# Kernel optimization log

Measured on AMD Instinct MI355X. Metric: run time of the kernel, lower is better.

The kernel has to match this reference:

```python
import jax, jax.numpy as jnp
import numpy as np

K = 12           # boundary_k
TEMP = 0.75      # logit_temperature


def _knn_idx(p):
    # p: [N,3]; brute-force kNN within one batch element (pointops offsets => per-batch)
    sq = jnp.sum(p * p, axis=-1)
    d2 = sq[:, None] + sq[None, :] - 2.0 * (p @ p.T)   # [N,N]
    _, idx = jax.lax.top_k(-d2, K + 1)                  # self is nearest (d=0)
    return idx[:, 1:]                                    # drop self -> [N,K]


def _mlp2(x, W1, b1, W2, b2, relu_out):
    h = jax.nn.relu(x @ W1 + b1) @ W2 + b2
    return jax.nn.relu(h) if relu_out else h


def setup_inputs() -> dict:
    key = jax.random.key(0)
    ks = jax.random.split(key, 32)
    B, N, C = 4, 4096, 17
    dims = [256, 512, 768]
    RD = 320
    s = 0.02
    inp = {
        'feat0': jax.random.normal(ks[0], (B, N, dims[0]), jnp.float32),
        'feat1': jax.random.normal(ks[1], (B, N, dims[1]), jnp.float32),
        'feat2': jax.random.normal(ks[2], (B, N, dims[2]), jnp.float32),
        'logits': jax.random.normal(ks[3], (B, N, C), jnp.float32),
        'labels': jax.random.randint(ks[4], (B, N), 0, C, jnp.int32),
        'pos': jax.random.normal(ks[5], (B, N, 3), jnp.float32),
    }
    # feat projections
    for i, d in enumerate(dims):
        inp[f'Wp{i}'] = jax.random.normal(ks[6 + i], (d, RD), jnp.float32) * s
        inp[f'bp{i}'] = jnp.zeros((RD,), jnp.float32)
    # boundary encoder 6->96->160
    inp['Wbe1'] = jax.random.normal(ks[10], (6, 96), jnp.float32) * s
    inp['bbe1'] = jnp.zeros((96,), jnp.float32)
    inp['Wbe2'] = jax.random.normal(ks[11], (96, 160), jnp.float32) * s
    inp['bbe2'] = jnp.zeros((160,), jnp.float32)
    # attention (RD+160)->320->n_scales
    inp['Wa1'] = jax.random.normal(ks[12], (RD + 160, 320), jnp.float32) * s
    inp['ba1'] = jnp.zeros((320,), jnp.float32)
    inp['Wa2'] = jax.random.normal(ks[13], (320, 3), jnp.float32) * s
    inp['ba2'] = jnp.zeros((3,), jnp.float32)
    # output proj RD->RD->RD
    inp['Wo1'] = jax.random.normal(ks[14], (RD, RD), jnp.float32) * s
    inp['bo1'] = jnp.zeros((RD,), jnp.float32)
    inp['Wo2'] = jax.random.normal(ks[15], (RD, RD), jnp.float32) * s
    inp['bo2'] = jnp.zeros((RD,), jnp.float32)
    return inp


def boundary_info(logits, labels, pos):
    idx = jax.vmap(_knn_idx)(pos)                          # [B,N,K]
    nb_lab = jax.vmap(lambda l, i: l[i])(labels, idx)      # [B,N,K]
    nb_pos = jax.vmap(lambda p, i: p[i])(pos, idx)         # [B,N,K,3]
    diff = nb_lab != labels[..., None]                     # [B,N,K]
    diff_f = diff.astype(jnp.float32)
    dist = jnp.linalg.norm(nb_pos - pos[:, :, None, :], axis=-1)  # [B,N,K]
    boundary_score = diff_f.mean(axis=-1)
    same = 1.0 - diff_f
    same_dist = (dist * same).sum(-1) / (same.sum(-1) + 1e-6)
    bdist = jnp.min(jnp.where(diff, dist, jnp.inf), axis=-1)
    bdist = jnp.where(jnp.isfinite(bdist), bdist, same_dist)
    mean_d = dist.mean(-1)
    density = 1.0 / (mean_d + 1e-6)
    curvature = jnp.std(dist, axis=-1, ddof=1) / (mean_d + 1e-6)  # torch.std unbiased
    probs = jax.nn.softmax(logits / TEMP, axis=-1)
    confidence = probs.max(-1)
    entropy = -(probs * jnp.log(probs + 1e-8)).sum(-1) / jnp.log(jnp.float32(probs.shape[-1]))
    return jnp.stack([boundary_score, confidence, entropy, density, curvature, bdist], axis=-1)


def reference(feat0, feat1, feat2, logits, labels, pos,
              Wp0, bp0, Wp1, bp1, Wp2, bp2,
              Wbe1, bbe1, Wbe2, bbe2,
              Wa1, ba1, Wa2, ba2,
              Wo1, bo1, Wo2, bo2):
    fp = jnp.stack([feat0 @ Wp0 + bp0, feat1 @ Wp1 + bp1, feat2 @ Wp2 + bp2], axis=2)  # [B,N,3,RD]
    info = boundary_info(logits, labels, pos)                       # [B,N,6]
    enc = _mlp2(info, Wbe1, bbe1, Wbe2, bbe2, relu_out=True)        # [B,N,160]
    global_feat = fp.mean(axis=2)                                   # [B,N,RD]
    attn_in = jnp.concatenate([global_feat, enc], axis=-1)
    attn = jax.nn.softmax(_mlp2(attn_in, Wa1, ba1, Wa2, ba2, relu_out=False), axis=-1)  # [B,N,3]
    fused = (fp * attn[..., None]).sum(axis=2)                      # [B,N,RD]
    out = _mlp2(fused, Wo1, bo1, Wo2, bo2, relu_out=False) + global_feat
    return out, attn
```

## Files before the change

kernel.cpp:

```cpp
#include <hip/hip_runtime.h>
#include <stdint.h>

typedef float fx4 __attribute__((ext_vector_type(4)));
typedef short s8 __attribute__((ext_vector_type(8)));
typedef short s4 __attribute__((ext_vector_type(4)));
typedef unsigned int u32;
typedef u32 ux4 __attribute__((ext_vector_type(4)));

#define MTOT 16384
#define NPTS 4096

#define VMCNT7 asm volatile("s_waitcnt vmcnt(7)" ::: "memory")
#define VMCNT5 asm volatile("s_waitcnt vmcnt(5)" ::: "memory")
#define VMCNT0 asm volatile("s_waitcnt vmcnt(0)" ::: "memory")
#define LGKM0  asm volatile("s_waitcnt lgkmcnt(0)" ::: "memory")
#define SBAR   asm volatile("s_barrier" ::: "memory")
#define SCHED0 __builtin_amdgcn_sched_barrier(0)

__device__ __forceinline__ float b2f(short s) {
    return __uint_as_float(((unsigned)(unsigned short)s) << 16);
}
__device__ __forceinline__ short f2b(float f) {
    unsigned u = __float_as_uint(f);
    u += 0x7fffu + ((u >> 16) & 1u);
    return (short)(u >> 16);
}
__device__ __forceinline__ void g2l16(const void* g, void* l) {
    __builtin_amdgcn_global_load_lds(
        (const __attribute__((address_space(1))) unsigned int*)g,
        (__attribute__((address_space(3))) unsigned int*)l, 16, 0, 0);
}
__device__ __forceinline__ void g2l4(const void* g, void* l) {
    __builtin_amdgcn_global_load_lds(
        (const __attribute__((address_space(1))) unsigned int*)g,
        (__attribute__((address_space(3))) unsigned int*)l, 4, 0, 0);
}

struct WTDesc {
    const float* W[8];
    short* Bt[8];
    int K[8];
    int N[8];
    int Kp[8];
    int swz[8];
    int base[9];
};

__global__ __launch_bounds__(256) void wtrans8_kernel(WTDesc d)
{
    int idx = blockIdx.x * 256 + threadIdx.x;
    if (idx >= d.base[8]) return;
    int s = 0;
#pragma unroll
    for (int t = 1; t < 8; ++t) if (idx >= d.base[t]) s = t;
    int local = idx - d.base[s];
    int N = d.N[s];
    if (d.swz[s]) {
        int c = local / 10240, r = local - c * 10240;
        int n = r >> 5, q = r & 31, slot = q >> 3, t = q & 7;
        int kl = ((slot ^ ((n >> 1) & 3)) << 3) | t;
        int k = c * 32 + kl;
        d.Bt[s][local] = f2b(d.W[s][(size_t)k * N + n]);
    } else {
        int Kp = d.Kp[s], K = d.K[s];
        int n = local / Kp, k = local - n * Kp;
        d.Bt[s][local] = (k < K) ? f2b(d.W[s][(size_t)k * N + n]) : (short)0;
    }
}

#define SEGW 132
#define KCAP 40

template<int K>
__device__ __forceinline__ void aprep_one(
    const float* __restrict__ src, short* __restrict__ dst, int aid)
{
    constexpr int KT8 = K * 4;
    int mtile = aid / KT8;
    int r8 = aid - mtile * KT8;
    int r2 = r8 * 8;
    int chunk = r2 >> 10;
    int within = r2 & 1023;
    int r = within >> 5, q = within & 31;
    int slot = q >> 3;
    int k = chunk * 32 + ((slot ^ ((r >> 1) & 3)) << 3);
    int row = mtile * 32 + r;
    const float* sp = src + (size_t)row * K + k;
    fx4 v0 = *(const fx4*)sp, v1 = *(const fx4*)(sp + 4);
    s8 o;
    o[0] = f2b(v0[0]); o[1] = f2b(v0[1]); o[2] = f2b(v0[2]); o[3] = f2b(v0[3]);
    o[4] = f2b(v1[0]); o[5] = f2b(v1[1]); o[6] = f2b(v1[2]); o[7] = f2b(v1[3]);
    *(s8*)(dst + (size_t)aid * 8) = o;
}

__global__ __launch_bounds__(512) void knap_kernel(
    const float* __restrict__ pos, u32* __restrict__ keys,
    const float* __restrict__ f0, const float* __restrict__ f1, const float* __restrict__ f2,
    short* __restrict__ a0, short* __restrict__ a1, short* __restrict__ a2)
{
    __shared__ float xs[8 * SEGW], ys[8 * SEGW], zs[8 * SEGW];
    __shared__ u32 cand[64 * KCAP];
    __shared__ u32 samp[64 * 16];
    __shared__ u32 tauA[64];
    __shared__ int cnt[64];

    int bid = blockIdx.x;
    if (bid >= 1024) {
        int g = (bid - 1024) * 512 + threadIdx.x;
        if (g < 1572864)      aprep_one<768>(f2, a2, g);
        else if (g < 2621440) aprep_one<512>(f1, a1, g - 1572864);
        else                  aprep_one<256>(f0, a0, g - 2621440);
        return;
    }

    int b   = bid >> 8;
    int cc  = (bid >> 6) & 3;
    int pch = bid & 63;
    int tid = threadIdx.x;
    int jb  = cc << 10;

    if (tid < 64) cnt[tid] = 0;
    for (int idx = tid; idx < 1024; idx += 512) {
        int seg = idx >> 7, o = idx & 127;
        const float* pp = pos + (size_t)(b * NPTS + jb + idx) * 3;
        xs[seg * SEGW + o] = pp[0];
        ys[seg * SEGW + o] = pp[1];
        zs[seg * SEGW + o] = pp[2];
    }
    __syncthreads();

    int lp = tid >> 3, q = tid & 7;
    int gi = pch * 64 + lp;
    const float* mp = pos + (size_t)(b * NPTS + gi) * 3;
    float mx = mp[0], my = mp[1], mz = mp[2];

    const float* xsq = xs + q * SEGW;
    const float* ysq = ys + q * SEGW;
    const float* zsq = zs + q * SEGW;
    int jg0 = jb + q * 128;

    u32 h0 = 0xFFFFFFFFu, h1v = 0xFFFFFFFFu;
    for (int jj = 0; jj < 128; jj += 4) {
        fx4 xv = *reinterpret_cast<const fx4*>(xsq + jj);
        fx4 yv = *reinterpret_cast<const fx4*>(ysq + jj);
        fx4 zv = *reinterpret_cast<const fx4*>(zsq + jj);
#pragma unroll
        for (int u = 0; u < 4; ++u) {
            float dx = xv[u] - mx, dy = yv[u] - my, dz = zv[u] - mz;
            float d2 = fmaf(dx, dx, fmaf(dy, dy, dz * dz));
            u32 d2m = __float_as_uint(d2) & 0xFFFFF000u;
            if (jg0 + jj + u == gi) d2m = 0xFFFFFFFFu;
            u32 lo = (d2m < h0) ? d2m : h0;
            u32 hi = (d2m < h0) ? h0 : d2m;
            h0 = lo;
            h1v = (hi < h1v) ? hi : h1v;
        }
    }
    u32 m0 = h0 | (u32)(q * 2);
    u32 m1 = h1v | (u32)(q * 2 + 1);
    samp[lp * 16 + q * 2]     = m0;
    samp[lp * 16 + q * 2 + 1] = m1;
    __syncthreads();

    {
        ux4 sv0 = *(ux4*)&samp[lp * 16];
        ux4 sv1 = *(ux4*)&samp[lp * 16 + 4];
        ux4 sv2 = *(ux4*)&samp[lp * 16 + 8];
        ux4 sv3 = *(ux4*)&samp[lp * 16 + 12];
        int r0 = 0, r1 = 0;
#pragma unroll
        for (int i = 0; i < 4; ++i) {
            r0 += (sv0[i] < m0) + (sv1[i] < m0) + (sv2[i] < m0) + (sv3[i] < m0);
            r1 += (sv0[i] < m1) + (sv1[i] < m1) + (sv2[i] < m1) + (sv3[i] < m1);
        }
        if (r0 == 11) tauA[lp] = m0;
        if (r1 == 11) tauA[lp] = m1;
    }
    __syncthreads();
    u32 tau = tauA[lp];

    for (int jj = 0; jj < 128; jj += 4) {
        fx4 xv = *reinterpret_cast<const fx4*>(xsq + jj);
        fx4 yv = *reinterpret_cast<const fx4*>(ysq + jj);
        fx4 zv = *reinterpret_cast<const fx4*>(zsq + jj);
#pragma unroll
        for (int u = 0; u < 4; ++u) {
            float dx = xv[u] - mx, dy = yv[u] - my, dz = zv[u] - mz;
            float d2 = fmaf(dx, dx, fmaf(dy, dy, dz * dz));
            int jg = jg0 + jj + u;
            u32 d2m = __float_as_uint(d2) & 0xFFFFF000u;
            if (jg == gi) d2m = 0xFFFFFFFFu;
            if (d2m <= tau) {
                int slot = atomicAdd(&cnt[lp], 1);
                if (slot < KCAP) cand[lp * KCAP + slot] = d2m | (u32)jg;
            }
        }
    }
    __syncthreads();

    int n = cnt[lp];
    u32 out[12];
    if (n <= KCAP) {
        u32 e0, e1, e2, e3, e4;
        e0 = (q      < n) ? cand[lp * KCAP + q]      : 0xFFFFFFFFu;
        e1 = (q + 8  < n) ? cand[lp * KCAP + q + 8]  : 0xFFFFFFFFu;
        e2 = (q + 16 < n) ? cand[lp * KCAP + q + 16] : 0xFFFFFFFFu;
        e3 = (q + 24 < n) ? cand[lp * KCAP + q + 24] : 0xFFFFFFFFu;
        e4 = (q + 32 < n) ? cand[lp * KCAP + q + 32] : 0xFFFFFFFFu;
#define CE(a, b) { u32 t0 = (a < b) ? a : b; u32 t1 = (a < b) ? b : a; a = t0; b = t1; }
        CE(e0, e1) CE(e1, e2) CE(e2, e3) CE(e3, e4)
        CE(e0, e1) CE(e1, e2) CE(e2, e3)
        CE(e0, e1) CE(e1, e2)
        CE(e0, e1)
#undef CE
        cand[lp * KCAP + q]      = e0;
        cand[lp * KCAP + q + 8]  = e1;
        cand[lp * KCAP + q + 16] = e2;
        cand[lp * KCAP + q + 24] = e3;
        cand[lp * KCAP + q + 32] = e4;
        int ptr = 0;
        u32 head = e0;
#pragma unroll
        for (int r = 0; r < 12; ++r) {
            u32 m = head;
            u32 o1 = __shfl_xor(m, 4, 8); m = (o1 < m) ? o1 : m;
            u32 o2 = __shfl_xor(m, 2, 8); m = (o2 < m) ? o2 : m;
            u32 o3 = __shfl_xor(m, 1, 8); m = (o3 < m) ? o3 : m;
            if (m == head) {
                ++ptr;
                head = (ptr < 5) ? cand[lp * KCAP + q + ptr * 8] : 0xFFFFFFFFu;
            }
            out[r] = m;
        }
    } else {
        u32 hk[12];
#pragma unroll
        for (int k = 0; k < 12; ++k) hk[k] = 0xFFFFFFFFu;
        for (int jj = 0; jj < 128; jj += 4) {
            fx4 xv = *reinterpret_cast<const fx4*>(xsq + jj);
            fx4 yv = *reinterpret_cast<const fx4*>(ysq + jj);
            fx4 zv = *reinterpret_cast<const fx4*>(zsq + jj);
#pragma unroll
            for (int u = 0; u < 4; ++u) {
                float dx = xv[u] - mx, dy = yv[u] - my, dz = zv[u] - mz;
                float d2 = fmaf(dx, dx, fmaf(dy, dy, dz * dz));
                int jg = jg0 + jj + u;
                u32 key = (__float_as_uint(d2) & 0xFFFFF000u) | (u32)jg;
                if (jg == gi) key = 0xFFFFFFFFu;
                if (key < hk[11]) {
                    hk[11] = key;
#pragma unroll
                    for (int k = 11; k >= 1; --k) {
                        u32 a = hk[k], bb = hk[k - 1];
                        u32 mn = (a < bb) ? a : bb;
                        u32 mxv = (a < bb) ? bb : a;
                        hk[k - 1] = mn; hk[k] = mxv;
                    }
                }
            }
        }
#pragma unroll
        for (int r = 0; r < 12; ++r) {
            u32 m = hk[0];
            u32 o1 = __shfl_xor(m, 4, 8); m = (o1 < m) ? o1 : m;
            u32 o2 = __shfl_xor(m, 2, 8); m = (o2 < m) ? o2 : m;
            u32 o3 = __shfl_xor(m, 1, 8); m = (o3 < m) ? o3 : m;
            if (m == hk[0]) {
#pragma unroll
                for (int k = 0; k < 11; ++k) hk[k] = hk[k + 1];
                hk[11] = 0xFFFFFFFFu;
            }
            out[r] = m;
        }
    }

    size_t kb = ((size_t)(b * NPTS + gi) * 4 + cc) * 12;
    if (q == 0) *reinterpret_cast<ux4*>(&keys[kb])     = (ux4){out[0], out[1], out[2], out[3]};
    if (q == 1) *reinterpret_cast<ux4*>(&keys[kb + 4]) = (ux4){out[4], out[5], out[6], out[7]};
    if (q == 2) *reinterpret_cast<ux4*>(&keys[kb + 8]) = (ux4){out[8], out[9], out[10], out[11]};
}

__global__ __launch_bounds__(256) void knn_merge_kernel(
    const u32* __restrict__ keys, const int* __restrict__ labels,
    const float* __restrict__ logits, float* __restrict__ info32)
{
    __shared__ unsigned char labs[NPTS];
    int b  = blockIdx.x >> 6;
    int pc = blockIdx.x & 63;
    int tid = threadIdx.x;
    for (int idx = tid; idx < NPTS; idx += 256)
        labs[idx] = (unsigned char)labels[b * NPTS + idx];
    __syncthreads();

    int lp = tid >> 2, q = tid & 3;
    int gi = pc * 64 + lp;
    size_t kb = ((size_t)(b * NPTS + gi) * 4 + q) * 12;
    ux4 k0 = *reinterpret_cast<const ux4*>(&keys[kb]);
    ux4 k1 = *reinterpret_cast<const ux4*>(&keys[kb + 4]);
    ux4 k2 = *reinterpret_cast<const ux4*>(&keys[kb + 8]);
    u32 hk[12];
    hk[0] = k0[0]; hk[1] = k0[1]; hk[2] = k0[2]; hk[3] = k0[3];
    hk[4] = k1[0]; hk[5] = k1[1]; hk[6] = k1[2]; hk[7] = k1[3];
    hk[8] = k2[0]; hk[9] = k2[1]; hk[10] = k2[2]; hk[11] = k2[3];

    int mylab = (int)labs[gi];
    float sum_d = 0.f, sum_d2 = 0.f, sum_diff = 0.f, same_d = 0.f, bmin = 3.0e38f;
#pragma unroll
    for (int r = 0; r < 12; ++r) {
        u32 m = hk[0];
        u32 o1 = __shfl_xor(m, 2, 4); m = (o1 < m) ? o1 : m;
        u32 o2 = __shfl_xor(m, 1, 4); m = (o2 < m) ? o2 : m;
        if (m == hk[0]) {
#pragma unroll
            for (int k = 0; k < 11; ++k) hk[k] = hk[k + 1];
            hk[11] = 0xFFFFFFFFu;
        }
        float d = sqrtf(__uint_as_float(m & 0xFFFFF000u));
        int j = (int)(m & 0xFFFu);
        float isdiff = ((int)labs[j] != mylab) ? 1.0f : 0.0f;
        sum_d += d;
        sum_d2 = fmaf(d, d, sum_d2);
        sum_diff += isdiff;
        same_d = fmaf(d, 1.0f - isdiff, same_d);
        if (isdiff > 0.f) bmin = fminf(bmin, d);
    }

    if (q == 0) {
        float nsame = 12.0f - sum_diff;
        float mean_d = sum_d * (1.0f / 12.0f);
        float var = fmaxf(0.f, (sum_d2 - 12.0f * mean_d * mean_d) * (1.0f / 11.0f));
        float md_eps = mean_d + 1e-6f;
        float curvature = sqrtf(var) / md_eps;
        float density = 1.0f / md_eps;
        float same_dist = same_d / (nsame + 1e-6f);
        float bdist = (bmin < 2.9e38f) ? bmin : same_dist;
        float bscore = sum_diff * (1.0f / 12.0f);

        const float* lg = logits + (size_t)(b * NPTS + gi) * 17;
        float v[17];
        float vmax = -3.0e38f;
#pragma unroll
        for (int c = 0; c < 17; ++c) { v[c] = lg[c] * (1.0f / 0.75f); vmax = fmaxf(vmax, v[c]); }
        float ssum = 0.f;
#pragma unroll
        for (int c = 0; c < 17; ++c) { v[c] = expf(v[c] - vmax); ssum += v[c]; }
        float inv = 1.0f / ssum;
        float conf = 0.f, ent = 0.f;
#pragma unroll
        for (int c = 0; c < 17; ++c) {
            float pprob = v[c] * inv;
            conf = fmaxf(conf, pprob);
            ent += pprob * logf(pprob + 1e-8f);
        }
        ent = -ent * (1.0f / 2.8332133f);

        float* op = info32 + (size_t)(b * NPTS + gi) * 32;
        fx4 o0 = {bscore, conf, ent, density};
        fx4 o1v = {curvature, bdist, 0.f, 0.f};
        fx4 zz = {0.f, 0.f, 0.f, 0.f};
        *reinterpret_cast<fx4*>(op + 0)  = o0;
        *reinterpret_cast<fx4*>(op + 4)  = o1v;
        *reinterpret_cast<fx4*>(op + 8)  = zz;
        *reinterpret_cast<fx4*>(op + 12) = zz;
        *reinterpret_cast<fx4*>(op + 16) = zz;
        *reinterpret_cast<fx4*>(op + 20) = zz;
        *reinterpret_cast<fx4*>(op + 24) = zz;
        *reinterpret_cast<fx4*>(op + 28) = zz;
    }
}

template<bool AF32, bool RELU, bool NMASK, bool ADDF, bool OUTF, bool OUTB>
__global__ __launch_bounds__(256) void gemm_k(
    const void* __restrict__ Ap, int lda,
    const short* __restrict__ Bt,
    const float* __restrict__ bias,
    float* __restrict__ Cf, int ldcf,
    short* __restrict__ Cb, int ldcb, int cboff,
    const float* __restrict__ Af, int ldaf,
    int N, int K, int ntiles)
{
    __shared__ short As[128 * 40];
    __shared__ short Bs[64 * 40];
    int bid = blockIdx.x;
    int mt = bid / ntiles, nt = bid - mt * ntiles;
    int m0 = mt * 128, n0 = nt * 64;
    int tid = threadIdx.x, l = tid & 63, wid = tid >> 6;
    int wm = wid & 1, wn = wid >> 1, lr = l & 15, lh = l >> 4;
    fx4 acc[4][2] = {};

    int nsteps = K >> 5;
    for (int kt = 0; kt < nsteps; ++kt) {
        int k0 = kt << 5;
        if constexpr (AF32) {
            const float* A = (const float*)Ap;
#pragma unroll
            for (int it = 0; it < 4; ++it) {
                int tt = tid + it * 256;
                int row = tt >> 3, seg = tt & 7;
                fx4 vv = *reinterpret_cast<const fx4*>(A + (size_t)(m0 + row) * lda + k0 + seg * 4);
                s4 w; w[0] = f2b(vv[0]); w[1] = f2b(vv[1]); w[2] = f2b(vv[2]); w[3] = f2b(vv[3]);
                *reinterpret_cast<s4*>(&As[row * 40 + seg * 4]) = w;
            }
        } else {
            const short* A = (const short*)Ap;
#pragma unroll
            for (int it = 0; it < 2; ++it) {
                int tt = tid + it * 256;
                int row = tt >> 2, seg = tt & 3;
                s8 vv = *reinterpret_cast<const s8*>(A + (size_t)(m0 + row) * lda + k0 + seg * 8);
                *reinterpret_cast<s8*>(&As[row * 40 + seg * 8]) = vv;
            }
        }
        {
            int row = tid >> 2, seg = tid & 3;
            s8 vb = {0, 0, 0, 0, 0, 0, 0, 0};
            if (!NMASK || (n0 + row) < N)
                vb = *reinterpret_cast<const s8*>(Bt + (size_t)(n0 + row) * K + k0 + seg * 8);
            *reinterpret_cast<s8*>(&Bs[row * 40 + seg * 8]) = vb;
        }
        __syncthreads();
        s8 af[4], bfr[2];
#pragma unroll
        for (int mf = 0; mf < 4; ++mf)
            af[mf] = *reinterpret_cast<s8*>(&As[(wm * 64 + mf * 16 + lr) * 40 + lh * 8]);
#pragma unroll
        for (int nf = 0; nf < 2; ++nf)
            bfr[nf] = *reinterpret_cast<s8*>(&Bs[(wn * 32 + nf * 16 + lr) * 40 + lh * 8]);
#pragma unroll
        for (int mf = 0; mf < 4; ++mf)
#pragma unroll
            for (int nf = 0; nf < 2; ++nf)
                acc[mf][nf] = __builtin_amdgcn_mfma_f32_16x16x32_bf16(af[mf], bfr[nf], acc[mf][nf], 0, 0, 0);
        __syncthreads();
    }

#pragma unroll
    for (int nf = 0; nf < 2; ++nf) {
        int col = n0 + wn * 32 + nf * 16 + lr;
        if (NMASK && col >= N) continue;
        float bv = bias[col];
#pragma unroll
        for (int mf = 0; mf < 4; ++mf) {
            int r0 = m0 + wm * 64 + mf * 16 + lh * 4;
#pragma unroll
            for (int rg = 0; rg < 4; ++rg) {
                float c = acc[mf][nf][rg] + bv;
                if (RELU) c = fmaxf(c, 0.0f);
                int row = r0 + rg;
                if constexpr (ADDF) c += Af[(size_t)row * ldaf + col];
                if constexpr (OUTF) Cf[(size_t)row * ldcf + col] = c;
                if constexpr (OUTB) Cb[(size_t)row * ldcb + cboff + col] = f2b(c);
            }
        }
    }
}

__global__ __launch_bounds__(256, 2) void mega_kernel(
    const short* __restrict__ at0, const short* __restrict__ at1, const short* __restrict__ at2,
    const short* __restrict__ btp0, const short* __restrict__ btp1, const short* __restrict__ btp2,
    const float* __restrict__ bp0, const float* __restrict__ bp1, const float* __restrict__ bp2,
    const short* __restrict__ bta1, const float* __restrict__ ba1,
    const float* __restrict__ Wa2, const float* __restrict__ ba2,
    const short* __restrict__ bto1, const float* __restrict__ bo1,
    const short* __restrict__ bto2, const float* __restrict__ bo2,
    const short* __restrict__ encb, short* __restrict__ fpb,
    float* __restrict__ outf, float* __restrict__ attn_out)
{
    __shared__ alignas(16) short smem[38144];
    char* smb = (char*)smem;
    constexpr int BB0 = 0, BB1 = 20480, AB0 = 40960, AB1 = 43008, R2B = 45056, SWF = 75776;
    constexpr size_t FPS = (size_t)512 * 256 * 40;
    float* smf = (float*)(smb + SWF);

    int tid = threadIdx.x, l = tid & 63, wid = tid >> 6;
    int lr = l & 15, lh = l >> 4;
    int m0 = blockIdx.x * 32;
    short* fpt = fpb + (size_t)(blockIdx.x * 256 + tid) * 40;

    auto stageB = [&](int bbase, const short* btg, int kt) {
#pragma unroll
        for (int r = 0; r < 5; ++r) {
            int idx = tid + r * 256;
            g2l16(btg + (size_t)kt * 10240 + idx * 8, smb + bbase + idx * 16);
        }
    };
    auto stageA = [&](int abase, const short* atgm, int kt) {
        const short* src = atgm + (size_t)kt * 1024;
        g2l4(src + tid * 2,       smb + abase + tid * 4);
        g2l4(src + 512 + tid * 2, smb + abase + 1024 + tid * 4);
    };
    auto readB = [&](int bbase, s8* bf) {
#pragma unroll
        for (int nf = 0; nf < 5; ++nf) {
            int row = wid * 80 + nf * 16 + lr;
            bf[nf] = *(const s8*)(smb + bbase + row * 64 + ((lh ^ ((row >> 1) & 3)) << 4));
        }
    };
    auto readAp = [&](int abase, s8* af) {
#pragma unroll
        for (int mf = 0; mf < 2; ++mf) {
            int row = mf * 16 + lr;
            af[mf] = *(const s8*)(smb + abase + row * 64 + ((lh ^ ((row >> 1) & 3)) << 4));
        }
    };

    fx4 gacc[2][5] = {};

    auto do_proj = [&](const short* atgm, const short* btg, int ns,
                       const float* bias, short* fpo) {
        fx4 acc[2][5] = {};
        stageB(BB0, btg, 0); stageA(AB0, atgm, 0);
        stageB(BB1, btg, 1); stageA(AB1, atgm, 1);
        LGKM0;
#pragma unroll 1
        for (int kt = 0; kt < ns; ++kt) {
            if (kt < ns - 1) { VMCNT7; } else { VMCNT0; }
            SBAR;
            int cb = (kt & 1) ? BB1 : BB0;
            int ca = (kt & 1) ? AB1 : AB0;
            s8 af[2], bf[5];
            readAp(ca, af);
            readB(cb, bf);
            LGKM0; SCHED0;
            SBAR;
            if (kt + 2 < ns) { stageB(cb, btg, kt + 2); stageA(ca, atgm, kt + 2); }
#pragma unroll
            for (int mf = 0; mf < 2; ++mf)
#pragma unroll
                for (int nf = 0; nf < 5; ++nf)
                    acc[mf][nf] = __builtin_amdgcn_mfma_f32_16x16x32_bf16(af[mf], bf[nf], acc[mf][nf], 0, 0, 0);
        }
#pragma unroll
        for (int nf = 0; nf < 5; ++nf) {
            float bv = bias[wid * 80 + nf * 16 + lr];
#pragma unroll
            for (int mf = 0; mf < 2; ++mf) {
                s4 pk;
#pragma unroll
                for (int rg = 0; rg < 4; ++rg) {
                    float c = acc[mf][nf][rg] + bv;
                    gacc[mf][nf][rg] += c;
                    pk[rg] = f2b(c);
                }
                *(s4*)(fpo + (mf * 5 + nf) * 4) = pk;
            }
        }
    };

    do_proj(at2 + (size_t)blockIdx.x * 24576, btp2, 24, bp2, fpt + 2 * FPS);
    do_proj(at1 + (size_t)blockIdx.x * 16384, btp1, 16, bp1, fpt + 1 * FPS);
    do_proj(at0 + (size_t)blockIdx.x * 8192,  btp0, 8,  bp0, fpt);

#pragma unroll
    for (int nf = 0; nf < 5; ++nf) {
        int col = wid * 80 + nf * 16 + lr;
#pragma unroll
        for (int mf = 0; mf < 2; ++mf)
#pragma unroll
            for (int rg = 0; rg < 4; ++rg) {
                int row = mf * 16 + lh * 4 + rg;
                int bir = (col * 2) ^ (((row >> 1) & 3) << 4);
                *(short*)(smb + R2B + row * 960 + bir) = f2b(gacc[mf][nf][rg] * (1.0f / 3.0f));
            }
    }
#pragma unroll
    for (int r = 0; r < 3; ++r) {
        int idx = tid + r * 256;
        if (idx < 640) {
            int row = idx / 20, sg = idx - row * 20;
            s8 v = *reinterpret_cast<const s8*>(encb + (size_t)(m0 + row) * 160 + sg * 8);
            int bir = (640 + sg * 16) ^ (((row >> 1) & 3) << 4);
            *(s8*)(smb + R2B + row * 960 + bir) = v;
        }
    }

    auto do_gemm2 = [&](const short* btg, int ns, fx4 (&acc)[2][5]) {
        stageB(BB0, btg, 0);
        stageB(BB1, btg, 1);
        LGKM0;
#pragma unroll 1
        for (int kt = 0; kt < ns; ++kt) {
            if (kt < ns - 1) { VMCNT5; } else { VMCNT0; }
            SBAR;
            int cb = (kt & 1) ? BB1 : BB0;
            s8 af[2], bf[5];
#pragma unroll
            for (int mf = 0; mf < 2; ++mf) {
                int row = mf * 16 + lr;
                int bir = (kt * 64 + (lh << 4)) ^ (((row >> 1) & 3) << 4);
                af[mf] = *(const s8*)(smb + R2B + row * 960 + bir);
            }
            readB(cb, bf);
            LGKM0; SCHED0;
            SBAR;
            if (kt + 2 < ns) stageB(cb, btg, kt + 2);
#pragma unroll
            for (int mf = 0; mf < 2; ++mf)
#pragma unroll
                for (int nf = 0; nf < 5; ++nf)
                    acc[mf][nf] = __builtin_amdgcn_mfma_f32_16x16x32_bf16(af[mf], bf[nf], acc[mf][nf], 0, 0, 0);
        }
    };

    {
        fx4 acc1[2][5] = {};
        do_gemm2(bta1, 15, acc1);
#pragma unroll
        for (int nf = 0; nf < 5; ++nf) {
            int col = wid * 80 + nf * 16 + lr;
            float bv = ba1[col];
#pragma unroll
            for (int mf = 0; mf < 2; ++mf)
#pragma unroll
                for (int rg = 0; rg < 4; ++rg) {
                    int row = mf * 16 + lh * 4 + rg;
                    int bir = (col * 2) ^ (((row >> 1) & 3) << 4);
                    *(short*)(smb + R2B + row * 960 + bir) = f2b(fmaxf(acc1[mf][nf][rg] + bv, 0.0f));
                }
        }
    }

    {
        float* ws2 = (float*)smb;
        if (tid < 240)
            reinterpret_cast<fx4*>(ws2)[tid] = reinterpret_cast<const fx4*>(Wa2)[tid];
        __syncthreads();
        int row = tid >> 3, g = tid & 7;
        float l0 = 0.f, l1 = 0.f, l2 = 0.f;
#pragma unroll
        for (int j = 0; j < 5; ++j) {
            int bir = (g * 80 + j * 16) ^ (((row >> 1) & 3) << 4);
            s8 v = *(const s8*)(smb + R2B + row * 960 + bir);
#pragma unroll
            for (int u = 0; u < 8; ++u) {
                float f = b2f(v[u]);
                const float* wp = ws2 + (g * 40 + j * 8 + u) * 3;
                l0 = fmaf(f, wp[0], l0);
                l1 = fmaf(f, wp[1], l1);
                l2 = fmaf(f, wp[2], l2);
            }
        }
#pragma unroll
        for (int s = 4; s >= 1; s >>= 1) {
            l0 += __shfl_xor(l0, s, 8);
            l1 += __shfl_xor(l1, s, 8);
            l2 += __shfl_xor(l2, s, 8);
        }
        if (g == 0) {
            l0 += ba2[0]; l1 += ba2[1]; l2 += ba2[2];
            float mx = fmaxf(l0, fmaxf(l1, l2));
            float e0 = expf(l0 - mx), e1 = expf(l1 - mx), e2 = expf(l2 - mx);
            float inv = 1.0f / (e0 + e1 + e2);
            float w0 = e0 * inv, w1 = e1 * inv, w2 = e2 * inv;
            attn_out[(size_t)(m0 + row) * 3 + 0] = w0;
            attn_out[(size_t)(m0 + row) * 3 + 1] = w1;
            attn_out[(size_t)(m0 + row) * 3 + 2] = w2;
            smf[row * 4 + 0] = w0; smf[row * 4 + 1] = w1; smf[row * 4 + 2] = w2;
        }
        __syncthreads();
    }

#pragma unroll
    for (int mf = 0; mf < 2; ++mf)
#pragma unroll
        for (int nf = 0; nf < 5; ++nf) {
            s4 p0 = *(const s4*)(fpt + (mf * 5 + nf) * 4);
            s4 p1 = *(const s4*)(fpt + 1 * FPS + (mf * 5 + nf) * 4);
            s4 p2 = *(const s4*)(fpt + 2 * FPS + (mf * 5 + nf) * 4);
            int col = wid * 80 + nf * 16 + lr;
#pragma unroll
            for (int rg = 0; rg < 4; ++rg) {
                int row = mf * 16 + lh * 4 + rg;
                float fv = smf[row * 4 + 0] * b2f(p0[rg])
                         + smf[row * 4 + 1] * b2f(p1[rg])
                         + smf[row * 4 + 2] * b2f(p2[rg]);
                int bir = (col * 2) ^ (((row >> 1) & 3) << 4);
                *(short*)(smb + R2B + row * 960 + bir) = f2b(fv);
            }
        }

    {
        fx4 acch[2][5] = {};
        do_gemm2(bto1, 10, acch);
#pragma unroll
        for (int nf = 0; nf < 5; ++nf) {
            int col = wid * 80 + nf * 16 + lr;
            float bv = bo1[col];
#pragma unroll
            for (int mf = 0; mf < 2; ++mf)
#pragma unroll
                for (int rg = 0; rg < 4; ++rg) {
                    int row = mf * 16 + lh * 4 + rg;
                    int bir = (col * 2) ^ (((row >> 1) & 3) << 4);
                    *(short*)(smb + R2B + row * 960 + bir) = f2b(fmaxf(acch[mf][nf][rg] + bv, 0.0f));
                }
        }
    }

    {
        fx4 acco[2][5] = {};
        do_gemm2(bto2, 10, acco);
#pragma unroll
        for (int nf = 0; nf < 5; ++nf) {
            int col = wid * 80 + nf * 16 + lr;
            float bv = bo2[col];
#pragma unroll
            for (int mf = 0; mf < 2; ++mf)
#pragma unroll
                for (int rg = 0; rg < 4; ++rg) {
                    int row = m0 + mf * 16 + lh * 4 + rg;
                    float c = acco[mf][nf][rg] + bv + gacc[mf][nf][rg] * (1.0f / 3.0f);
                    outf[(size_t)row * 320 + col] = c;
                }
        }
    }
}

extern "C" void kernel_launch(void* const* d_in, const int* in_sizes, int n_in,
                              void* d_out, int out_size, void* d_ws, size_t ws_size,
                              hipStream_t stream)
{
    const float* feat0  = (const float*)d_in[0];
    const float* feat1  = (const float*)d_in[1];
    const float* feat2  = (const float*)d_in[2];
    const float* logits = (const float*)d_in[3];
    const int*   labels = (const int*)d_in[4];
    const float* pos    = (const float*)d_in[5];
    const float* Wp0 = (const float*)d_in[6];   const float* bp0 = (const float*)d_in[7];
    const float* Wp1 = (const float*)d_in[8];   const float* bp1 = (const float*)d_in[9];
    const float* Wp2 = (const float*)d_in[10];  const float* bp2 = (const float*)d_in[11];
    const float* Wbe1 = (const float*)d_in[12]; const float* bbe1 = (const float*)d_in[13];
    const float* Wbe2 = (const float*)d_in[14]; const float* bbe2 = (const float*)d_in[15];
    const float* Wa1 = (const float*)d_in[16];  const float* ba1 = (const float*)d_in[17];
    const float* Wa2 = (const float*)d_in[18];  const float* ba2 = (const float*)d_in[19];
    const float* Wo1 = (const float*)d_in[20];  const float* bo1 = (const float*)d_in[21];
    const float* Wo2 = (const float*)d_in[22];  const float* bo2 = (const float*)d_in[23];

    char* p = (char*)d_ws;
    auto alloc = [&](size_t bytes) { char* r = p; p += (bytes + 255) & ~(size_t)255; return r; };
    short* bt_p0  = (short*)alloc((size_t)320 * 256 * 2);
    short* bt_p1  = (short*)alloc((size_t)320 * 512 * 2);
    short* bt_p2  = (short*)alloc((size_t)320 * 768 * 2);
    short* bt_be1 = (short*)alloc((size_t)96 * 32 * 2);
    short* bt_be2 = (short*)alloc((size_t)160 * 96 * 2);
    short* bt_a1  = (short*)alloc((size_t)320 * 480 * 2);
    short* bt_o1  = (short*)alloc((size_t)320 * 320 * 2);
    short* bt_o2  = (short*)alloc((size_t)320 * 320 * 2);
    float* info32 = (float*)alloc((size_t)MTOT * 32 * 4);
    short* h1     = (short*)alloc((size_t)MTOT * 96 * 2);
    short* encb   = (short*)alloc((size_t)MTOT * 160 * 2);
    u32*   knnkeys= (u32*)alloc((size_t)MTOT * 4 * 12 * 4);
    short* abt0   = (short*)alloc((size_t)MTOT * 256 * 2);
    short* abt1   = (short*)alloc((size_t)MTOT * 512 * 2);
    short* abt2   = (short*)alloc((size_t)MTOT * 768 * 2);
    short* fpb    = (short*)alloc((size_t)3 * 512 * 256 * 40 * 2);

    float* outf = (float*)d_out;
    float* attn_out = outf + (size_t)MTOT * 320;

    WTDesc wd;
    const float* Ws[8] = {Wp0, Wp1, Wp2, Wbe1, Wbe2, Wa1, Wo1, Wo2};
    short* Bts[8] = {bt_p0, bt_p1, bt_p2, bt_be1, bt_be2, bt_a1, bt_o1, bt_o2};
    int Ks[8]  = {256, 512, 768, 6, 96, 480, 320, 320};
    int Ns[8]  = {320, 320, 320, 96, 160, 320, 320, 320};
    int Kps[8] = {256, 512, 768, 32, 96, 480, 320, 320};
    int Sz[8]  = {1, 1, 1, 0, 0, 1, 1, 1};
    int acc = 0;
    for (int s = 0; s < 8; ++s) {
        wd.W[s] = Ws[s]; wd.Bt[s] = Bts[s];
        wd.K[s] = Ks[s]; wd.N[s] = Ns[s]; wd.Kp[s] = Kps[s]; wd.swz[s] = Sz[s];
        wd.base[s] = acc;
        acc += Ns[s] * Kps[s];
    }
    wd.base[8] = acc;
    wtrans8_kernel<<<(acc + 255) / 256, 256, 0, stream>>>(wd);

    knap_kernel<<<7168, 512, 0, stream>>>(pos, knnkeys,
                                          feat0, feat1, feat2,
                                          abt0, abt1, abt2);
    knn_merge_kernel<<<256, 256, 0, stream>>>(knnkeys, labels, logits, info32);

    gemm_k<true, true, true, false, false, true><<<256, 256, 0, stream>>>(
        info32, 32, bt_be1, bbe1, nullptr, 0, h1, 96, 0, nullptr, 0, 96, 32, 2);
    gemm_k<false, true, true, false, false, true><<<384, 256, 0, stream>>>(
        h1, 96, bt_be2, bbe2, nullptr, 0, encb, 160, 0, nullptr, 0, 160, 96, 3);

    mega_kernel<<<512, 256, 0, stream>>>(
        abt0, abt1, abt2,
        bt_p0, bt_p1, bt_p2,
        bp0, bp1, bp2,
        bt_a1, ba1, Wa2, ba2,
        bt_o1, bo1, bt_o2, bo2,
        encb, fpb, outf, attn_out);
}
```

Measured before the change: 131.8 us.

## Use 512-thread blocks in mega_kernel with 2x4 warp tiling

Raises mega_kernel from 256 to 512 threads per block and arranges the 8 waves as 2 (M) x 4 (N), so each wave computes one 16-row fragment instead of two. The B and A staging loads are respread across the larger thread count, the vmcnt waits are adjusted to match, and the per-thread fp scratch layout shrinks to 20 shorts. The goal is more waves per CU to hide latency and fewer accumulator registers per thread. In exchange each wave does less MFMA work per LDS B-fragment read and the barriers cover more waves.

```diff
diff --git a/kernel.cpp b/kernel.cpp
--- a/kernel.cpp
+++ b/kernel.cpp
@@ -10,8 +10,8 @@
 #define MTOT 16384
 #define NPTS 4096
 
-#define VMCNT7 asm volatile("s_waitcnt vmcnt(7)" ::: "memory")
 #define VMCNT5 asm volatile("s_waitcnt vmcnt(5)" ::: "memory")
+#define VMCNT4 asm volatile("s_waitcnt vmcnt(4)" ::: "memory")
 #define VMCNT0 asm volatile("s_waitcnt vmcnt(0)" ::: "memory")
 #define LGKM0  asm volatile("s_waitcnt lgkmcnt(0)" ::: "memory")
 #define SBAR   asm volatile("s_barrier" ::: "memory")
@@ -455,7 +455,7 @@
     }
 }
 
-__global__ __launch_bounds__(256, 2) void mega_kernel(
+__global__ __launch_bounds__(512, 2) void mega_kernel(
     const short* __restrict__ at0, const short* __restrict__ at1, const short* __restrict__ at2,
     const short* __restrict__ btp0, const short* __restrict__ btp1, const short* __restrict__ btp2,
     const float* __restrict__ bp0, const float* __restrict__ bp1, const float* __restrict__ bp2,
@@ -469,154 +469,141 @@
     __shared__ alignas(16) short smem[38144];
     char* smb = (char*)smem;
     constexpr int BB0 = 0, BB1 = 20480, AB0 = 40960, AB1 = 43008, R2B = 45056, SWF = 75776;
-    constexpr size_t FPS = (size_t)512 * 256 * 40;
+    constexpr size_t FPS = (size_t)512 * 512 * 20;
     float* smf = (float*)(smb + SWF);
 
-    int tid = threadIdx.x, l = tid & 63, wid = tid >> 6;
-    int lr = l & 15, lh = l >> 4;
+    int tid = threadIdx.x, wid = tid >> 6, l = tid & 63;
+    int wm = wid >> 2, wn = wid & 3, lr = l & 15, lh = l >> 4;
     int m0 = blockIdx.x * 32;
-    short* fpt = fpb + (size_t)(blockIdx.x * 256 + tid) * 40;
+    short* fpt = fpb + (size_t)(blockIdx.x * 512 + tid) * 20;
 
     auto stageB = [&](int bbase, const short* btg, int kt) {
-#pragma unroll
-        for (int r = 0; r < 5; ++r) {
-            int idx = tid + r * 256;
-            g2l16(btg + (size_t)kt * 10240 + idx * 8, smb + bbase + idx * 16);
-        }
+        const char* s = (const char*)(btg + (size_t)kt * 10240);
+        int o1 = tid * 16;
+        int o2 = 8192 + tid * 16;
+        int o3 = 16384 + tid * 4;
+        int o4 = 18432 + tid * 4;
+        g2l16(s + o1, smb + bbase + o1);
+        g2l16(s + o2, smb + bbase + o2);
+        g2l4(s + o3, smb + bbase + o3);
+        g2l4(s + o4, smb + bbase + o4);
     };
     auto stageA = [&](int abase, const short* atgm, int kt) {
-        const short* src = atgm + (size_t)kt * 1024;
-        g2l4(src + tid * 2,       smb + abase + tid * 4);
-        g2l4(src + 512 + tid * 2, smb + abase + 1024 + tid * 4);
+        const char* s = (const char*)(atgm + (size_t)kt * 1024);
+        g2l4(s + tid * 4, smb + abase + tid * 4);
     };
     auto readB = [&](int bbase, s8* bf) {
 #pragma unroll
         for (int nf = 0; nf < 5; ++nf) {
-            int row = wid * 80 + nf * 16 + lr;
+            int row = wn * 80 + nf * 16 + lr;
             bf[nf] = *(const s8*)(smb + bbase + row * 64 + ((lh ^ ((row >> 1) & 3)) << 4));
         }
     };
-    auto readAp = [&](int abase, s8* af) {
-#pragma unroll
-        for (int mf = 0; mf < 2; ++mf) {
-            int row = mf * 16 + lr;
-            af[mf] = *(const s8*)(smb + abase + row * 64 + ((lh ^ ((row >> 1) & 3)) << 4));
-        }
-    };
-
-    fx4 gacc[2][5] = {};
+
+    fx4 gacc[5] = {};
 
     auto do_proj = [&](const short* atgm, const short* btg, int ns,
                        const float* bias, short* fpo) {
-        fx4 acc[2][5] = {};
+        fx4 acc[5] = {};
         stageB(BB0, btg, 0); stageA(AB0, atgm, 0);
         stageB(BB1, btg, 1); stageA(AB1, atgm, 1);
-        LGKM0;
-#pragma unroll 1
-        for (int kt = 0; kt < ns; ++kt) {
-            if (kt < ns - 1) { VMCNT7; } else { VMCNT0; }
-            SBAR;
-            int cb = (kt & 1) ? BB1 : BB0;
-            int ca = (kt & 1) ? AB1 : AB0;
-            s8 af[2], bf[5];
-            readAp(ca, af);
-            readB(cb, bf);
-            LGKM0; SCHED0;
-            SBAR;
-            if (kt + 2 < ns) { stageB(cb, btg, kt + 2); stageA(ca, atgm, kt + 2); }
-#pragma unroll
-            for (int mf = 0; mf < 2; ++mf)
-#pragma unroll
-                for (int nf = 0; nf < 5; ++nf)
-                    acc[mf][nf] = __builtin_amdgcn_mfma_f32_16x16x32_bf16(af[mf], bf[nf], acc[mf][nf], 0, 0, 0);
-        }
-#pragma unroll
-        for (int nf = 0; nf < 5; ++nf) {
-            float bv = bias[wid * 80 + nf * 16 + lr];
-#pragma unroll
-            for (int mf = 0; mf < 2; ++mf) {
-                s4 pk;
-#pragma unroll
-                for (int rg = 0; rg < 4; ++rg) {
-                    float c = acc[mf][nf][rg] + bv;
-                    gacc[mf][nf][rg] += c;
-                    pk[rg] = f2b(c);
-                }
-                *(s4*)(fpo + (mf * 5 + nf) * 4) = pk;
-            }
-        }
-    };
-
-    do_proj(at2 + (size_t)blockIdx.x * 24576, btp2, 24, bp2, fpt + 2 * FPS);
-    do_proj(at1 + (size_t)blockIdx.x * 16384, btp1, 16, bp1, fpt + 1 * FPS);
-    do_proj(at0 + (size_t)blockIdx.x * 8192,  btp0, 8,  bp0, fpt);
-
-#pragma unroll
-    for (int nf = 0; nf < 5; ++nf) {
-        int col = wid * 80 + nf * 16 + lr;
-#pragma unroll
-        for (int mf = 0; mf < 2; ++mf)
-#pragma unroll
-            for (int rg = 0; rg < 4; ++rg) {
-                int row = mf * 16 + lh * 4 + rg;
-                int bir = (col * 2) ^ (((row >> 1) & 3) << 4);
-                *(short*)(smb + R2B + row * 960 + bir) = f2b(gacc[mf][nf][rg] * (1.0f / 3.0f));
-            }
-    }
-#pragma unroll
-    for (int r = 0; r < 3; ++r) {
-        int idx = tid + r * 256;
-        if (idx < 640) {
-            int row = idx / 20, sg = idx - row * 20;
-            s8 v = *reinterpret_cast<const s8*>(encb + (size_t)(m0 + row) * 160 + sg * 8);
-            int bir = (640 + sg * 16) ^ (((row >> 1) & 3) << 4);
-            *(s8*)(smb + R2B + row * 960 + bir) = v;
-        }
-    }
-
-    auto do_gemm2 = [&](const short* btg, int ns, fx4 (&acc)[2][5]) {
-        stageB(BB0, btg, 0);
-        stageB(BB1, btg, 1);
         LGKM0;
 #pragma unroll 1
         for (int kt = 0; kt < ns; ++kt) {
             if (kt < ns - 1) { VMCNT5; } else { VMCNT0; }
             SBAR;
             int cb = (kt & 1) ? BB1 : BB0;
-            s8 af[2], bf[5];
-#pragma unroll
-            for (int mf = 0; mf < 2; ++mf) {
-                int row = mf * 16 + lr;
+            int ca = (kt & 1) ? AB1 : AB0;
+            s8 af, bf[5];
+            {
+                int row = wm * 16 + lr;
+                af = *(const s8*)(smb + ca + row * 64 + ((lh ^ ((row >> 1) & 3)) << 4));
+            }
+            readB(cb, bf);
+            LGKM0; SCHED0;
+            SBAR;
+            if (kt + 2 < ns) { stageB(cb, btg, kt + 2); stageA(ca, atgm, kt + 2); }
+#pragma unroll
+            for (int nf = 0; nf < 5; ++nf)
+                acc[nf] = __builtin_amdgcn_mfma_f32_16x16x32_bf16(af, bf[nf], acc[nf], 0, 0, 0);
+        }
+#pragma unroll
+        for (int nf = 0; nf < 5; ++nf) {
+            float bv = bias[wn * 80 + nf * 16 + lr];
+            s4 pk;
+#pragma unroll
+            for (int rg = 0; rg < 4; ++rg) {
+                float c = acc[nf][rg] + bv;
+                gacc[nf][rg] += c;
+                pk[rg] = f2b(c);
+            }
+            *(s4*)(fpo + nf * 4) = pk;
+        }
+    };
+
+    do_proj(at2 + (size_t)blockIdx.x * 24576, btp2, 24, bp2, fpt + 2 * FPS);
+    do_proj(at1 + (size_t)blockIdx.x * 16384, btp1, 16, bp1, fpt + 1 * FPS);
+    do_proj(at0 + (size_t)blockIdx.x * 8192,  btp0, 8,  bp0, fpt);
+
+#pragma unroll
+    for (int nf = 0; nf < 5; ++nf) {
+        int col = wn * 80 + nf * 16 + lr;
+#pragma unroll
+        for (int rg = 0; rg < 4; ++rg) {
+            int row = wm * 16 + lh * 4 + rg;
+            int bir = (col * 2) ^ (((row >> 1) & 3) << 4);
+            *(short*)(smb + R2B + row * 960 + bir) = f2b(gacc[nf][rg] * (1.0f / 3.0f));
+        }
+    }
+#pragma unroll
+    for (int r = 0; r < 2; ++r) {
+        int idx = tid + r * 512;
+        if (idx < 640) {
+            int row = idx / 20, sg = idx - row * 20;
+            s8 v = *reinterpret_cast<const s8*>(encb + (size_t)(m0 + row) * 160 + sg * 8);
+            int bir = (640 + sg * 16) ^ (((row >> 1) & 3) << 4);
+            *(s8*)(smb + R2B + row * 960 + bir) = v;
+        }
+    }
+
+    auto do_gemm2 = [&](const short* btg, int ns, fx4 (&acc)[5]) {
+        stageB(BB0, btg, 0);
+        stageB(BB1, btg, 1);
+        LGKM0;
+#pragma unroll 1
+        for (int kt = 0; kt < ns; ++kt) {
+            if (kt < ns - 1) { VMCNT4; } else { VMCNT0; }
+            SBAR;
+            int cb = (kt & 1) ? BB1 : BB0;
+            s8 af, bf[5];
+            {
+                int row = wm * 16 + lr;
                 int bir = (kt * 64 + (lh << 4)) ^ (((row >> 1) & 3) << 4);
-                af[mf] = *(const s8*)(smb + R2B + row * 960 + bir);
+                af = *(const s8*)(smb + R2B + row * 960 + bir);
             }
             readB(cb, bf);
             LGKM0; SCHED0;
             SBAR;
             if (kt + 2 < ns) stageB(cb, btg, kt + 2);
 #pragma unroll
-            for (int mf = 0; mf < 2; ++mf)
-#pragma unroll
-                for (int nf = 0; nf < 5; ++nf)
-                    acc[mf][nf] = __builtin_amdgcn_mfma_f32_16x16x32_bf16(af[mf], bf[nf], acc[mf][nf], 0, 0, 0);
+            for (int nf = 0; nf < 5; ++nf)
+                acc[nf] = __builtin_amdgcn_mfma_f32_16x16x32_bf16(af, bf[nf], acc[nf], 0, 0, 0);
         }
     };
 
     {
-        fx4 acc1[2][5] = {};
+        fx4 acc1[5] = {};
         do_gemm2(bta1, 15, acc1);
 #pragma unroll
         for (int nf = 0; nf < 5; ++nf) {
-            int col = wid * 80 + nf * 16 + lr;
+            int col = wn * 80 + nf * 16 + lr;
             float bv = ba1[col];
 #pragma unroll
-            for (int mf = 0; mf < 2; ++mf)
-#pragma unroll
-                for (int rg = 0; rg < 4; ++rg) {
-                    int row = mf * 16 + lh * 4 + rg;
-                    int bir = (col * 2) ^ (((row >> 1) & 3) << 4);
-                    *(short*)(smb + R2B + row * 960 + bir) = f2b(fmaxf(acc1[mf][nf][rg] + bv, 0.0f));
-                }
+            for (int rg = 0; rg < 4; ++rg) {
+                int row = wm * 16 + lh * 4 + rg;
+                int bir = (col * 2) ^ (((row >> 1) & 3) << 4);
+                *(short*)(smb + R2B + row * 960 + bir) = f2b(fmaxf(acc1[nf][rg] + bv, 0.0f));
+            }
         }
     }
 
@@ -625,93 +612,89 @@
         if (tid < 240)
             reinterpret_cast<fx4*>(ws2)[tid] = reinterpret_cast<const fx4*>(Wa2)[tid];
         __syncthreads();
-        int row = tid >> 3, g = tid & 7;
-        float l0 = 0.f, l1 = 0.f, l2 = 0.f;
-#pragma unroll
-        for (int j = 0; j < 5; ++j) {
-            int bir = (g * 80 + j * 16) ^ (((row >> 1) & 3) << 4);
-            s8 v = *(const s8*)(smb + R2B + row * 960 + bir);
-#pragma unroll
-            for (int u = 0; u < 8; ++u) {
-                float f = b2f(v[u]);
-                const float* wp = ws2 + (g * 40 + j * 8 + u) * 3;
-                l0 = fmaf(f, wp[0], l0);
-                l1 = fmaf(f, wp[1], l1);
-                l2 = fmaf(f, wp[2], l2);
-            }
-        }
-#pragma unroll
-        for (int s = 4; s >= 1; s >>= 1) {
-            l0 += __shfl_xor(l0, s, 8);
-            l1 += __shfl_xor(l1, s, 8);
-            l2 += __shfl_xor(l2, s, 8);
-        }
-        if (g == 0) {
-            l0 += ba2[0]; l1 += ba2[1]; l2 += ba2[2];
-            float mx = fmaxf(l0, fmaxf(l1, l2));
-            float e0 = expf(l0 - mx), e1 = expf(l1 - mx), e2 = expf(l2 - mx);
-            float inv = 1.0f / (e0 + e1 + e2);
-            float w0 = e0 * inv, w1 = e1 * inv, w2 = e2 * inv;
-            attn_out[(size_t)(m0 + row) * 3 + 0] = w0;
-            attn_out[(size_t)(m0 + row) * 3 + 1] = w1;
-            attn_out[(size_t)(m0 + row) * 3 + 2] = w2;
-            smf[row * 4 + 0] = w0; smf[row * 4 + 1] = w1; smf[row * 4 + 2] = w2;
+        if (tid < 256) {
+            int row = tid >> 3, g = tid & 7;
+            float l0 = 0.f, l1 = 0.f, l2 = 0.f;
+#pragma unroll
+            for (int j = 0; j < 5; ++j) {
+                int bir = (g * 80 + j * 16) ^ (((row >> 1) & 3) << 4);
+                s8 v = *(const s8*)(smb + R2B + row * 960 + bir);
+#pragma unroll
+                for (int u = 0; u < 8; ++u) {
+                    float f = b2f(v[u]);
+                    const float* wp = ws2 + (g * 40 + j * 8 + u) * 3;
+                    l0 = fmaf(f, wp[0], l0);
+                    l1 = fmaf(f, wp[1], l1);
+                    l2 = fmaf(f, wp[2], l2);
+                }
+            }
+#pragma unroll
+            for (int s = 4; s >= 1; s >>= 1) {
+                l0 += __shfl_xor(l0, s, 8);
+                l1 += __shfl_xor(l1, s, 8);
+                l2 += __shfl_xor(l2, s, 8);
+            }
+            if (g == 0) {
+                l0 += ba2[0]; l1 += ba2[1]; l2 += ba2[2];
+                float mx = fmaxf(l0, fmaxf(l1, l2));
+                float e0 = expf(l0 - mx), e1 = expf(l1 - mx), e2 = expf(l2 - mx);
+                float inv = 1.0f / (e0 + e1 + e2);
+                float w0 = e0 * inv, w1 = e1 * inv, w2 = e2 * inv;
+                attn_out[(size_t)(m0 + row) * 3 + 0] = w0;
+                attn_out[(size_t)(m0 + row) * 3 + 1] = w1;
+                attn_out[(size_t)(m0 + row) * 3 + 2] = w2;
+                smf[row * 4 + 0] = w0; smf[row * 4 + 1] = w1; smf[row * 4 + 2] = w2;
+            }
         }
         __syncthreads();
     }
 
 #pragma unroll
-    for (int mf = 0; mf < 2; ++mf)
+    for (int nf = 0; nf < 5; ++nf) {
+        s4 p0 = *(const s4*)(fpt + nf * 4);
+        s4 p1 = *(const s4*)(fpt + 1 * FPS + nf * 4);
+        s4 p2 = *(const s4*)(fpt + 2 * FPS + nf * 4);
+        int col = wn * 80 + nf * 16 + lr;
+#pragma unroll
+        for (int rg = 0; rg < 4; ++rg) {
+            int row = wm * 16 + lh * 4 + rg;
+            float fv = smf[row * 4 + 0] * b2f(p0[rg])
+                     + smf[row * 4 + 1] * b2f(p1[rg])
+                     + smf[row * 4 + 2] * b2f(p2[rg]);
+            int bir = (col * 2) ^ (((row >> 1) & 3) << 4);
+            *(short*)(smb + R2B + row * 960 + bir) = f2b(fv);
+        }
+    }
+
+    {
+        fx4 acch[5] = {};
+        do_gemm2(bto1, 10, acch);
 #pragma unroll
         for (int nf = 0; nf < 5; ++nf) {
-            s4 p0 = *(const s4*)(fpt + (mf * 5 + nf) * 4);
-            s4 p1 = *(const s4*)(fpt + 1 * FPS + (mf * 5 + nf) * 4);
-            s4 p2 = *(const s4*)(fpt + 2 * FPS + (mf * 5 + nf) * 4);
-            int col = wid * 80 + nf * 16 + lr;
+            int col = wn * 80 + nf * 16 + lr;
+            float bv = bo1[col];
 #pragma unroll
             for (int rg = 0; rg < 4; ++rg) {
-                int row = mf * 16 + lh * 4 + rg;
-                float fv = smf[row * 4 + 0] * b2f(p0[rg])
-                         + smf[row * 4 + 1] * b2f(p1[rg])
-                         + smf[row * 4 + 2] * b2f(p2[rg]);
+                int row = wm * 16 + lh * 4 + rg;
                 int bir = (col * 2) ^ (((row >> 1) & 3) << 4);
-                *(short*)(smb + R2B + row * 960 + bir) = f2b(fv);
-            }
-        }
+                *(short*)(smb + R2B + row * 960 + bir) = f2b(fmaxf(acch[nf][rg] + bv, 0.0f));
+            }
+        }
+    }
 
     {
-        fx4 acch[2][5] = {};
-        do_gemm2(bto1, 10, acch);
+        fx4 acco[5] = {};
+        do_gemm2(bto2, 10, acco);
 #pragma unroll
         for (int nf = 0; nf < 5; ++nf) {
-            int col = wid * 80 + nf * 16 + lr;
-            float bv = bo1[col];
-#pragma unroll
-            for (int mf = 0; mf < 2; ++mf)
-#pragma unroll
-                for (int rg = 0; rg < 4; ++rg) {
-                    int row = mf * 16 + lh * 4 + rg;
-                    int bir = (col * 2) ^ (((row >> 1) & 3) << 4);
-                    *(short*)(smb + R2B + row * 960 + bir) = f2b(fmaxf(acch[mf][nf][rg] + bv, 0.0f));
-                }
-        }
-    }
-
-    {
-        fx4 acco[2][5] = {};
-        do_gemm2(bto2, 10, acco);
-#pragma unroll
-        for (int nf = 0; nf < 5; ++nf) {
-            int col = wid * 80 + nf * 16 + lr;
+            int col = wn * 80 + nf * 16 + lr;
             float bv = bo2[col];
 #pragma unroll
-            for (int mf = 0; mf < 2; ++mf)
-#pragma unroll
-                for (int rg = 0; rg < 4; ++rg) {
-                    int row = m0 + mf * 16 + lh * 4 + rg;
-                    float c = acco[mf][nf][rg] + bv + gacc[mf][nf][rg] * (1.0f / 3.0f);
-                    outf[(size_t)row * 320 + col] = c;
-                }
+            for (int rg = 0; rg < 4; ++rg) {
+                int row = m0 + wm * 16 + lh * 4 + rg;
+                float c = acco[nf][rg] + bv + gacc[nf][rg] * (1.0f / 3.0f);
+                outf[(size_t)row * 320 + col] = c;
+            }
         }
     }
 }
@@ -753,7 +736,7 @@
     short* abt0   = (short*)alloc((size_t)MTOT * 256 * 2);
     short* abt1   = (short*)alloc((size_t)MTOT * 512 * 2);
     short* abt2   = (short*)alloc((size_t)MTOT * 768 * 2);
-    short* fpb    = (short*)alloc((size_t)3 * 512 * 256 * 40 * 2);
+    short* fpb    = (short*)alloc((size_t)3 * 512 * 512 * 20 * 2);
 
     float* outf = (float*)d_out;
     float* attn_out = outf + (size_t)MTOT * 320;
@@ -785,7 +768,7 @@
     gemm_k<false, true, true, false, false, true><<<384, 256, 0, stream>>>(
         h1, 96, bt_be2, bbe2, nullptr, 0, encb, 160, 0, nullptr, 0, 160, 96, 3);
 
-    mega_kernel<<<512, 256, 0, stream>>>(
+    mega_kernel<<<512, 512, 0, stream>>>(
         abt0, abt1, abt2,
         bt_p0, bt_p1, bt_p2,
         bp0, bp1, bp2,
```

New measurement: 167.5 us. +27.1%, slower.
